# Kernel tuning notes

Hardware: AMD Instinct MI355X
Metric: run time of the kernel (lower is better)

## Reference

```python
import jax, jax.numpy as jnp
import numpy as np
from jax import lax

N = 51200            # total nodes
E = 409600           # edges
FEAT = 768           # BERT emb size
HID = 256            # GGNN out_channels
L = 6                # GGNN layers
NPG = 200            # nodes per graph (conv1d_1 in_channels)
C1_OUT, K1, P1 = 50, 3, 1
C2_OUT, K2 = 20, 1
MP1_K, MP1_S = 3, 2
MP2_K, MP2_S = 2, 2

def _pooled_len(n):
    n = (n - MP1_K) // MP1_S + 1
    n = (n - MP2_K) // MP2_S + 1
    return n

def setup_inputs():
    key = jax.random.key(0)
    ks = jax.random.split(key, 12)
    s = lambda i, shape: jax.random.normal(ks[i], shape, jnp.float32) * 0.02
    fc1_in = C2_OUT * _pooled_len(HID + FEAT)  # 20*255 = 5100
    fc2_in = C2_OUT * _pooled_len(HID)         # 20*63  = 1260
    return dict(
        x=jax.random.normal(ks[0], (N, FEAT), jnp.float32),
        edge_index=jax.random.randint(ks[1], (2, E), 0, N, dtype=jnp.int32),
        W_in=s(2, (HID, FEAT)), b_in=jnp.zeros((HID,), jnp.float32),
        W_ggnn=s(3, (L, HID, HID)),
        W_ih=s(4, (3 * HID, HID)), W_hh=s(5, (3 * HID, HID)),
        b_ih=jnp.zeros((3 * HID,), jnp.float32), b_hh=jnp.zeros((3 * HID,), jnp.float32),
        Wc1=s(6, (C1_OUT, NPG, K1)), bc1=jnp.zeros((C1_OUT,), jnp.float32),
        Wc2=s(7, (C2_OUT, C1_OUT, K2)), bc2=jnp.zeros((C2_OUT,), jnp.float32),
        Wf1=s(8, (1, fc1_in)), bf1=jnp.zeros((1,), jnp.float32),
        Wf2=s(9, (1, fc2_in)), bf2=jnp.zeros((1,), jnp.float32),
    )

def _conv1d(x, w, b, pad):
    y = lax.conv_general_dilated(x, w, (1,), [(pad, pad)], dimension_numbers=('NCH', 'OIH', 'NCH'))
    return y + b[None, :, None]

def _maxpool1d(x, k, s):
    return lax.reduce_window(x, -jnp.inf, lax.max, (1, 1, k), (1, 1, s), 'VALID')

def _ggnn(h0, src, dst, W_ggnn, W_ih, W_hh, b_ih, b_hh):
    h = h0
    for i in range(L):  # fixed small layer loop
        m = h @ W_ggnn[i]                                   # [N, HID]
        agg = jax.ops.segment_sum(m[src], dst, num_segments=N)  # scatter-add aggr
        gi = agg @ W_ih.T + b_ih                            # GRUCell input gates
        gh = h @ W_hh.T + b_hh                              # GRUCell hidden gates
        i_r, i_z, i_n = jnp.split(gi, 3, axis=1)
        h_r, h_z, h_n = jnp.split(gh, 3, axis=1)
        r = jax.nn.sigmoid(i_r + h_r)
        z = jax.nn.sigmoid(i_z + h_z)
        n = jnp.tanh(i_n + r * h_n)
        h = (1.0 - z) * n + z * h
    return h

def _conv_head(h, x, Wc1, bc1, Wc2, bc2, Wf1, bf1, Wf2, bf2):
    concat = jnp.concatenate([h, x], axis=1).reshape(-1, NPG, HID + FEAT)  # [G, NPG, 1024]
    Z = _maxpool1d(jax.nn.relu(_conv1d(concat, Wc1, bc1, P1)), MP1_K, MP1_S)
    Z = _maxpool1d(_conv1d(Z, Wc2, bc2, 0), MP2_K, MP2_S)
    Y = h.reshape(-1, NPG, HID)
    Y = _maxpool1d(jax.nn.relu(_conv1d(Y, Wc1, bc1, P1)), MP1_K, MP1_S)
    Y = _maxpool1d(_conv1d(Y, Wc2, bc2, 0), MP2_K, MP2_S)
    z = Z.reshape(Z.shape[0], -1) @ Wf1.T + bf1
    y = Y.reshape(Y.shape[0], -1) @ Wf2.T + bf2
    # dropout p=0.2 is identity in eval mode
    return jax.nn.sigmoid((z * y).ravel())  # [G]

def reference(x, edge_index, W_in, b_in, W_ggnn, W_ih, W_hh, b_ih, b_hh, Wc1, bc1, Wc2, bc2, Wf1, bf1, Wf2, bf2):
    h0 = x @ W_in.T + b_in
    h = _ggnn(h0, edge_index[0], edge_index[1], W_ggnn, W_ih, W_hh, b_ih, b_hh)
    p = _conv_head(h, x, Wc1, bc1, Wc2, bc2, Wf1, bf1, Wf2, bf2)
    eps = 1e-6
    p = jnp.clip(p, eps, 1.0 - eps)
    z1 = jnp.log(p / (1.0 - p))
    return jnp.stack([jnp.zeros_like(z1), z1], axis=1)  # [G, 2]
```

## Files before the change

### kernel.cpp

```cpp
#include <hip/hip_runtime.h>
#include <math.h>

#define N_NODES 51200
#define N_EDGES 409600
#define FEAT    768
#define HID     256
#define NPG     200
#define G_GRAPHS 256

typedef _Float16 f16x8 __attribute__((ext_vector_type(8)));
typedef _Float16 f16x4 __attribute__((ext_vector_type(4)));
typedef float    f32x4 __attribute__((ext_vector_type(4)));

__device__ __forceinline__ void cvt4(const float* __restrict__ in, _Float16* __restrict__ out, int i) {
    float4 v = *(const float4*)&in[i * 4];
    f16x4 h;
    h[0] = (_Float16)v.x; h[1] = (_Float16)v.y; h[2] = (_Float16)v.z; h[3] = (_Float16)v.w;
    *(f16x4*)&out[i * 4] = h;
}

__global__ __launch_bounds__(256) void k_prep(const float* __restrict__ W_in, const float* __restrict__ W_ih,
                                              const float* __restrict__ W_hh, const float* __restrict__ W_g,
                                              const float* __restrict__ x, const float* __restrict__ Wc1,
                                              const float* __restrict__ bih, const float* __restrict__ bhh,
                                              _Float16* __restrict__ Win_h, _Float16* __restrict__ Wih_h,
                                              _Float16* __restrict__ Whh_h, _Float16* __restrict__ Wg_h,
                                              _Float16* __restrict__ XF, _Float16* __restrict__ Wp,
                                              float* __restrict__ brz, float* __restrict__ bnn,
                                              _Float16* __restrict__ Wrz2,
                                              int* __restrict__ deg, int* __restrict__ fill) {
    int id = blockIdx.x * 256 + threadIdx.x;
    if (id < 49152) { cvt4(W_in, Win_h, id); return; }
    id -= 49152;
    if (id < 49152) { cvt4(W_ih, Wih_h, id); return; }
    id -= 49152;
    if (id < 49152) { cvt4(W_hh, Whh_h, id); return; }
    id -= 49152;
    if (id < 98304) { cvt4(W_g, Wg_h, id); return; }
    id -= 98304;
    if (id < 49152) {
        int ch = id / 12288, r = id - ch * 12288;
        int o = r / 192, k = r - o * 192;
        int dk = k >> 6, cc = k & 63;
        int c = ch * 64 + cc;
        float v = 0.f;
        if (o < 50 && c < NPG) v = Wc1[(o * NPG + c) * 3 + dk];
        Wp[id] = (_Float16)v;
        return;
    }
    id -= 49152;
    if (id < 1024) {
        if (id < 512) brz[id] = bih[id] + bhh[id];
        else {
            int q = id - 512;
            bnn[q] = (q < 256) ? bih[512 + q] : bhh[512 + (q - 256)];
        }
        return;
    }
    id -= 1024;
    if (id < 786432) {
        int l = id >> 17, r = id & 131071;
        int j = r >> 8, c = r & 255;
        Wrz2[(size_t)l * 262144 + j * 512 + 256 + c] = (_Float16)W_hh[j * 256 + c];
        return;
    }
    id -= 786432;
    if (id < 12800) { *(int4*)&deg[id * 4] = make_int4(0, 0, 0, 0); return; }
    id -= 12800;
    if (id < 12800) { *(int4*)&fill[id * 4] = make_int4(0, 0, 0, 0); return; }
    id -= 12800;
    if (id < 9830400) { cvt4(x, XF, id); return; }
}

__global__ __launch_bounds__(256) void k_deg(const int* __restrict__ ei, int* __restrict__ deg) {
    int e = blockIdx.x * 256 + threadIdx.x;
    if (e < N_EDGES) atomicAdd(&deg[ei[N_EDGES + e]], 1);
}

__global__ __launch_bounds__(1024) void k_scan(const int* __restrict__ deg, int* __restrict__ rowp) {
    __shared__ int sums[1024];
    int tid = threadIdx.x;
    int base = tid * 50;
    int s = 0;
    for (int j = 0; j < 50; ++j) s += deg[base + j];
    sums[tid] = s;
    __syncthreads();
    for (int off = 1; off < 1024; off <<= 1) {
        int v = 0;
        if (tid >= off) v = sums[tid - off];
        __syncthreads();
        sums[tid] += v;
        __syncthreads();
    }
    int run = sums[tid] - s;
    for (int j = 0; j < 50; ++j) { rowp[base + j] = run; run += deg[base + j]; }
    if (tid == 1023) rowp[N_NODES] = run;
}

__global__ __launch_bounds__(256) void k_fill(const int* __restrict__ ei, const int* __restrict__ rowp,
                                              int* __restrict__ fill, int* __restrict__ col) {
    int e = blockIdx.x * 256 + threadIdx.x;
    if (e < N_EDGES) {
        int d = ei[N_EDGES + e];
        int pos = atomicAdd(&fill[d], 1);
        col[rowp[d] + pos] = ei[e];
    }
}

template<int AF16, int OUT, int COLB, int SWZ>
__global__ __launch_bounds__(256) void k_gemm2(const void* __restrict__ Av, int lda,
                                               const _Float16* __restrict__ B,
                                               const float* __restrict__ bias,
                                               void* __restrict__ Cv, int ldc,
                                               int K, int wgPerL, int aLStride, int bLStride,
                                               int cLStride, int biasStride) {
    __shared__ _Float16 As[128 * 64];
    __shared__ _Float16 Bs[128 * 64];
    int wg = blockIdx.x;
    int l = wg / wgPerL; wg -= l * wgPerL;
    if (AF16) Av = (const void*)((const _Float16*)Av + (size_t)l * aLStride);
    else      Av = (const void*)((const float*)Av + (size_t)l * aLStride);
    B += (size_t)l * bLStride;
    if (bias) bias += (size_t)l * biasStride;
    if (OUT == 1) Cv = (void*)((_Float16*)Cv + (size_t)l * cLStride);
    else          Cv = (void*)((float*)Cv + (size_t)l * cLStride);
    int rowBase, colBase;
    if (SWZ) {
        int xcd = wg & 7, t = wg >> 3;
        int cb = t % COLB, gidx = t / COLB;
        rowBase = (gidx * 8 + xcd) * 128;
        colBase = cb * 128;
    } else {
        rowBase = (wg / COLB) * 128;
        colBase = (wg % COLB) * 128;
    }
    int tid = threadIdx.x;
    int lane = tid & 63;
    int wid = tid >> 6;
    int wr = wid >> 1, wc = wid & 1;
    f32x4 acc[4][4] = {};
    for (int k0 = 0; k0 < K; k0 += 64) {
        __syncthreads();
        #pragma unroll
        for (int p = 0; p < 4; ++p) {
            int c = p * 256 + tid;
            int row = c >> 3, slot = c & 7;
            int dst = row * 64 + ((slot ^ (row & 7)) * 8);
            if (AF16) {
                const _Float16* srcA = (const _Float16*)Av + (size_t)(rowBase + row) * lda + k0 + slot * 8;
                *(f16x8*)&As[dst] = *(const f16x8*)srcA;
            } else {
                const float* srcA = (const float*)Av + (size_t)(rowBase + row) * lda + k0 + slot * 8;
                float4 f0 = *(const float4*)srcA;
                float4 f1 = *(const float4*)(srcA + 4);
                f16x8 hv;
                hv[0] = (_Float16)f0.x; hv[1] = (_Float16)f0.y; hv[2] = (_Float16)f0.z; hv[3] = (_Float16)f0.w;
                hv[4] = (_Float16)f1.x; hv[5] = (_Float16)f1.y; hv[6] = (_Float16)f1.z; hv[7] = (_Float16)f1.w;
                *(f16x8*)&As[dst] = hv;
            }
            const _Float16* srcB = B + (size_t)(colBase + row) * K + k0 + slot * 8;
            *(f16x8*)&Bs[dst] = *(const f16x8*)srcB;
        }
        __syncthreads();
        #pragma unroll
        for (int ks = 0; ks < 2; ++ks) {
            f16x8 af[4], bf[4];
            #pragma unroll
            for (int mi = 0; mi < 4; ++mi) {
                int row = wr * 64 + mi * 16 + (lane & 15);
                int slot = (lane >> 4) + ks * 4;
                af[mi] = *(const f16x8*)&As[row * 64 + ((slot ^ (row & 7)) * 8)];
            }
            #pragma unroll
            for (int nj = 0; nj < 4; ++nj) {
                int row = wc * 64 + nj * 16 + (lane & 15);
                int slot = (lane >> 4) + ks * 4;
                bf[nj] = *(const f16x8*)&Bs[row * 64 + ((slot ^ (row & 7)) * 8)];
            }
            #pragma unroll
            for (int mi = 0; mi < 4; ++mi)
                #pragma unroll
                for (int nj = 0; nj < 4; ++nj)
                    acc[mi][nj] = __builtin_amdgcn_mfma_f32_16x16x32_f16(af[mi], bf[nj], acc[mi][nj], 0, 0, 0);
        }
    }
    #pragma unroll
    for (int mi = 0; mi < 4; ++mi) {
        #pragma unroll
        for (int nj = 0; nj < 4; ++nj) {
            int col = colBase + wc * 64 + nj * 16 + (lane & 15);
            float bv = bias ? bias[col] : 0.f;
            #pragma unroll
            for (int r = 0; r < 4; ++r) {
                int row = rowBase + wr * 64 + mi * 16 + (lane >> 4) * 4 + r;
                float val = acc[mi][nj][r] + bv;
                if (OUT == 0) ((float*)Cv)[(size_t)row * ldc + col] = val;
                else          ((_Float16*)Cv)[(size_t)row * ldc + col] = (_Float16)val;
            }
        }
    }
}

__global__ __launch_bounds__(256) void k_gemmrz(const _Float16* __restrict__ S, const _Float16* __restrict__ hc,
                                                const _Float16* __restrict__ B, const float* __restrict__ bias,
                                                _Float16* __restrict__ C) {
    __shared__ _Float16 As[128 * 64];
    __shared__ _Float16 Bs[128 * 64];
    int wg = blockIdx.x;
    int xcd = wg & 7, t = wg >> 3;
    int cb = t % 4, gidx = t / 4;
    int rowBase = (gidx * 8 + xcd) * 128;
    int colBase = cb * 128;
    int tid = threadIdx.x;
    int lane = tid & 63;
    int wid = tid >> 6;
    int wr = wid >> 1, wc = wid & 1;
    f32x4 acc[4][4] = {};
    for (int k0 = 0; k0 < 512; k0 += 64) {
        const _Float16* Abase = (k0 < 256) ? S : hc;
        int kk = k0 & 255;
        __syncthreads();
        #pragma unroll
        for (int p = 0; p < 4; ++p) {
            int c = p * 256 + tid;
            int row = c >> 3, slot = c & 7;
            int dst = row * 64 + ((slot ^ (row & 7)) * 8);
            *(f16x8*)&As[dst] = *(const f16x8*)&Abase[(size_t)(rowBase + row) * 256 + kk + slot * 8];
            *(f16x8*)&Bs[dst] = *(const f16x8*)&B[(size_t)(colBase + row) * 512 + k0 + slot * 8];
        }
        __syncthreads();
        #pragma unroll
        for (int ks = 0; ks < 2; ++ks) {
            f16x8 af[4], bf[4];
            #pragma unroll
            for (int mi = 0; mi < 4; ++mi) {
                int row = wr * 64 + mi * 16 + (lane & 15);
                int slot = (lane >> 4) + ks * 4;
                af[mi] = *(const f16x8*)&As[row * 64 + ((slot ^ (row & 7)) * 8)];
            }
            #pragma unroll
            for (int nj = 0; nj < 4; ++nj) {
                int row = wc * 64 + nj * 16 + (lane & 15);
                int slot = (lane >> 4) + ks * 4;
                bf[nj] = *(const f16x8*)&Bs[row * 64 + ((slot ^ (row & 7)) * 8)];
            }
            #pragma unroll
            for (int mi = 0; mi < 4; ++mi)
                #pragma unroll
                for (int nj = 0; nj < 4; ++nj)
                    acc[mi][nj] = __builtin_amdgcn_mfma_f32_16x16x32_f16(af[mi], bf[nj], acc[mi][nj], 0, 0, 0);
        }
    }
    #pragma unroll
    for (int mi = 0; mi < 4; ++mi) {
        #pragma unroll
        for (int nj = 0; nj < 4; ++nj) {
            int col = colBase + wc * 64 + nj * 16 + (lane & 15);
            float bv = bias[col];
            #pragma unroll
            for (int r = 0; r < 4; ++r) {
                int row = rowBase + wr * 64 + mi * 16 + (lane >> 4) * 4 + r;
                C[(size_t)row * 512 + col] = (_Float16)(acc[mi][nj][r] + bv);
            }
        }
    }
}

__global__ __launch_bounds__(512) void k_nngru(const _Float16* __restrict__ S, const _Float16* __restrict__ hc,
                                               const _Float16* __restrict__ B0, const _Float16* __restrict__ B1,
                                               const float* __restrict__ bnn, const _Float16* __restrict__ rz,
                                               _Float16* __restrict__ hn) {
    __shared__ _Float16 As0[128 * 64], As1[128 * 64], Bs0[128 * 64], Bs1[128 * 64];
    int wg = blockIdx.x;
    int xcd = wg & 7, t = wg >> 3;
    int cb = t % 2, gidx = t / 2;
    int rowBase = (gidx * 8 + xcd) * 128;
    int colBase = cb * 128;
    int tid = threadIdx.x;
    int lane = tid & 63;
    int wid = tid >> 6;
    int wr = wid >> 2, wc = wid & 3;
    f32x4 acc0[4][2] = {}, acc1[4][2] = {};
    for (int k0 = 0; k0 < 256; k0 += 64) {
        __syncthreads();
        #pragma unroll
        for (int p = 0; p < 8; ++p) {
            int q = p * 512 + tid;
            int tile = q >> 10;
            int c = q & 1023;
            int row = c >> 3, slot = c & 7;
            int dst = row * 64 + ((slot ^ (row & 7)) * 8);
            const _Float16* src;
            _Float16* d;
            if (tile == 0)      { src = S  + (size_t)(rowBase + row) * 256 + k0 + slot * 8; d = As0; }
            else if (tile == 1) { src = hc + (size_t)(rowBase + row) * 256 + k0 + slot * 8; d = As1; }
            else if (tile == 2) { src = B0 + (size_t)(colBase + row) * 256 + k0 + slot * 8; d = Bs0; }
            else                { src = B1 + (size_t)(colBase + row) * 256 + k0 + slot * 8; d = Bs1; }
            *(f16x8*)&d[dst] = *(const f16x8*)src;
        }
        __syncthreads();
        #pragma unroll
        for (int ks = 0; ks < 2; ++ks) {
            f16x8 a0[4], a1[4], b0[2], b1[2];
            #pragma unroll
            for (int mi = 0; mi < 4; ++mi) {
                int row = wr * 64 + mi * 16 + (lane & 15);
                int slot = (lane >> 4) + ks * 4;
                int off = row * 64 + ((slot ^ (row & 7)) * 8);
                a0[mi] = *(const f16x8*)&As0[off];
                a1[mi] = *(const f16x8*)&As1[off];
            }
            #pragma unroll
            for (int nj = 0; nj < 2; ++nj) {
                int row = wc * 32 + nj * 16 + (lane & 15);
                int slot = (lane >> 4) + ks * 4;
                int off = row * 64 + ((slot ^ (row & 7)) * 8);
                b0[nj] = *(const f16x8*)&Bs0[off];
                b1[nj] = *(const f16x8*)&Bs1[off];
            }
            #pragma unroll
            for (int mi = 0; mi < 4; ++mi)
                #pragma unroll
                for (int nj = 0; nj < 2; ++nj) {
                    acc0[mi][nj] = __builtin_amdgcn_mfma_f32_16x16x32_f16(a0[mi], b0[nj], acc0[mi][nj], 0, 0, 0);
                    acc1[mi][nj] = __builtin_amdgcn_mfma_f32_16x16x32_f16(a1[mi], b1[nj], acc1[mi][nj], 0, 0, 0);
                }
        }
    }
    #pragma unroll
    for (int mi = 0; mi < 4; ++mi) {
        #pragma unroll
        for (int nj = 0; nj < 2; ++nj) {
            int col = colBase + wc * 32 + nj * 16 + (lane & 15);
            float bi = bnn[col], bh = bnn[256 + col];
            #pragma unroll
            for (int r = 0; r < 4; ++r) {
                int row = rowBase + wr * 64 + mi * 16 + (lane >> 4) * 4 + r;
                float rv = (float)rz[(size_t)row * 512 + col];
                float zv = (float)rz[(size_t)row * 512 + 256 + col];
                float rg = 1.f / (1.f + expf(-rv));
                float zg = 1.f / (1.f + expf(-zv));
                float ng = tanhf((acc0[mi][nj][r] + bi) + rg * (acc1[mi][nj][r] + bh));
                float ho = (float)hc[(size_t)row * 256 + col];
                hn[(size_t)row * 256 + col] = (_Float16)((1.f - zg) * ng + zg * ho);
            }
        }
    }
}

__global__ __launch_bounds__(256) void k_agg5(const int* __restrict__ rowp, const int* __restrict__ col,
                                              const _Float16* __restrict__ hc, _Float16* __restrict__ S) {
    int v = blockIdx.x * 8 + (threadIdx.x >> 5);
    int lane = threadIdx.x & 31;
    int beg = rowp[v], end = rowp[v + 1];
    const _Float16* hf = hc + lane * 8;
    float a0 = 0.f, a1 = 0.f, a2 = 0.f, a3 = 0.f, a4 = 0.f, a5 = 0.f, a6 = 0.f, a7 = 0.f;
    int i = beg;
    for (; i + 3 < end; i += 4) {
        int c0 = col[i], c1 = col[i + 1], c2 = col[i + 2], c3 = col[i + 3];
        f16x8 u0 = *(const f16x8*)&hf[(size_t)c0 * 256];
        f16x8 u1 = *(const f16x8*)&hf[(size_t)c1 * 256];
        f16x8 u2 = *(const f16x8*)&hf[(size_t)c2 * 256];
        f16x8 u3 = *(const f16x8*)&hf[(size_t)c3 * 256];
        a0 += ((float)u0[0] + (float)u1[0]) + ((float)u2[0] + (float)u3[0]);
        a1 += ((float)u0[1] + (float)u1[1]) + ((float)u2[1] + (float)u3[1]);
        a2 += ((float)u0[2] + (float)u1[2]) + ((float)u2[2] + (float)u3[2]);
        a3 += ((float)u0[3] + (float)u1[3]) + ((float)u2[3] + (float)u3[3]);
        a4 += ((float)u0[4] + (float)u1[4]) + ((float)u2[4] + (float)u3[4]);
        a5 += ((float)u0[5] + (float)u1[5]) + ((float)u2[5] + (float)u3[5]);
        a6 += ((float)u0[6] + (float)u1[6]) + ((float)u2[6] + (float)u3[6]);
        a7 += ((float)u0[7] + (float)u1[7]) + ((float)u2[7] + (float)u3[7]);
    }
    for (; i < end; ++i) {
        f16x8 u = *(const f16x8*)&hf[(size_t)col[i] * 256];
        a0 += (float)u[0]; a1 += (float)u[1]; a2 += (float)u[2]; a3 += (float)u[3];
        a4 += (float)u[4]; a5 += (float)u[5]; a6 += (float)u[6]; a7 += (float)u[7];
    }
    f16x8 o;
    o[0] = (_Float16)a0; o[1] = (_Float16)a1; o[2] = (_Float16)a2; o[3] = (_Float16)a3;
    o[4] = (_Float16)a4; o[5] = (_Float16)a5; o[6] = (_Float16)a6; o[7] = (_Float16)a7;
    *(f16x8*)&S[(size_t)v * 256 + lane * 8] = o;
}

__global__ __launch_bounds__(256, 2) void k_conv1m(const _Float16* __restrict__ hf, const _Float16* __restrict__ xf,
                                                   const _Float16* __restrict__ Wp, const float* __restrict__ bc1,
                                                   float* __restrict__ outZ, float* __restrict__ outY) {
    __shared__ _Float16 XT[272 * 64];
    __shared__ _Float16 WL[64 * 192];
    int b = blockIdx.x;
    int g, t0, H;
    float* out;
    if (b < 1024) { g = b >> 2; t0 = (b & 3) * 256; H = 1024; out = outZ; }
    else          { g = b - 1024; t0 = 0; H = 256; out = outY; }
    int tid = threadIdx.x;
    int lane = tid & 63;
    int wn = (tid >> 6) * 64;
    f32x4 acc[4][4] = {};
    for (int ch = 0; ch < 4; ++ch) {
        __syncthreads();
        #pragma unroll
        for (int i = 0; i < 6; ++i) {
            int q = i * 256 + tid;
            int o = q / 24, sk = q - o * 24;
            int skp = (sk & 0x18) | ((sk & 7) ^ (o & 7));
            *(f16x8*)&WL[o * 192 + skp * 8] = *(const f16x8*)&Wp[ch * 12288 + o * 192 + sk * 8];
        }
        for (int u = tid; u < 272; u += 256) {
            int r8 = u / 34, pc = u - r8 * 34;
            int gstart = t0 - 8 + pc * 8;
            int c0 = r8 * 8;
            f16x8 zv;
            #pragma unroll
            for (int q = 0; q < 8; ++q) zv[q] = (_Float16)0.f;
            f16x8 rows[8];
            if (gstart < 0 || gstart >= H) {
                #pragma unroll
                for (int j = 0; j < 8; ++j) rows[j] = zv;
            } else {
                const _Float16* base;
                int stride;
                if (gstart < HID) { base = hf + gstart; stride = 256; }
                else              { base = xf + (gstart - HID); stride = 768; }
                int node0 = g * NPG + ch * 64 + c0;
                #pragma unroll
                for (int j = 0; j < 8; ++j) {
                    int cg = ch * 64 + c0 + j;
                    rows[j] = (cg < NPG) ? *(const f16x8*)&base[(size_t)(node0 + j) * stride] : zv;
                }
            }
            #pragma unroll
            for (int jj = 0; jj < 8; ++jj) {
                f16x8 w;
                #pragma unroll
                for (int j = 0; j < 8; ++j) w[j] = rows[j][jj];
                int p = pc * 8 + jj;
                int slot = r8 ^ jj ^ (pc & 7);
                *(f16x8*)&XT[p * 64 + slot * 8] = w;
            }
        }
        __syncthreads();
        #pragma unroll
        for (int ks = 0; ks < 6; ++ks) {
            int dk = ks >> 1, cs0 = (ks & 1) << 2;
            f16x8 af[4], bf[4];
            #pragma unroll
            for (int mi = 0; mi < 4; ++mi) {
                int o = mi * 16 + (lane & 15);
                int sk = ks * 4 + (lane >> 4);
                int skp = (sk & 0x18) | ((sk & 7) ^ (o & 7));
                af[mi] = *(const f16x8*)&WL[o * 192 + skp * 8];
            }
            #pragma unroll
            for (int nj = 0; nj < 4; ++nj) {
                int tw = wn + nj * 16 + (lane & 15) + dk + 7;
                int sp = (cs0 + (lane >> 4)) ^ (tw & 7) ^ ((tw >> 3) & 7);
                bf[nj] = *(const f16x8*)&XT[tw * 64 + sp * 8];
            }
            #pragma unroll
            for (int mi = 0; mi < 4; ++mi)
                #pragma unroll
                for (int nj = 0; nj < 4; ++nj)
                    acc[mi][nj] = __builtin_amdgcn_mfma_f32_16x16x32_f16(af[mi], bf[nj], acc[mi][nj], 0, 0, 0);
        }
    }
    #pragma unroll
    for (int mi = 0; mi < 4; ++mi) {
        #pragma unroll
        for (int r = 0; r < 4; ++r) {
            int o = mi * 16 + (lane >> 4) * 4 + r;
            if (o < 50) {
                float bv = bc1[o];
                #pragma unroll
                for (int nj = 0; nj < 4; ++nj) {
                    int t = t0 + wn + nj * 16 + (lane & 15);
                    float v = acc[mi][nj][r] + bv;
                    out[(size_t)g * 50 * H + (size_t)o * H + t] = v > 0.f ? v : 0.f;
                }
            }
        }
    }
}

__global__ __launch_bounds__(256) void k_pool1(const float* __restrict__ C1Z, const float* __restrict__ C1Y,
                                               float* __restrict__ P1Z, float* __restrict__ P1Y) {
    int b = blockIdx.x;
    const float* in;
    float* out;
    int H, U, go;
    if (b < 12800) { in = C1Z; out = P1Z; H = 1024; U = 511; go = b; }
    else           { in = C1Y; out = P1Y; H = 256;  U = 127; go = b - 12800; }
    const float* p = in + (size_t)go * H;
    float* q = out + (size_t)go * U;
    for (int u = threadIdx.x; u < U; u += 256) {
        float a = p[2 * u], bb = p[2 * u + 1], c = p[2 * u + 2];
        float mm = a > bb ? a : bb;
        q[u] = mm > c ? mm : c;
    }
}

__global__ __launch_bounds__(256) void k_c2p2(const float* __restrict__ P1Z, const float* __restrict__ P1Y,
                                              const float* __restrict__ Wc2, const float* __restrict__ bc2,
                                              float* __restrict__ P2Z, float* __restrict__ P2Y) {
    int g = blockIdx.x, oy = blockIdx.y;
    const float* P1;
    float* out;
    int U, U2, o2;
    if (oy < 20) { P1 = P1Z; out = P2Z; U = 511; U2 = 255; o2 = oy; }
    else         { P1 = P1Y; out = P2Y; U = 127; U2 = 63;  o2 = oy - 20; }
    float b = bc2[o2];
    for (int u2 = threadIdx.x; u2 < U2; u2 += 256) {
        float a0 = b, a1 = b;
        #pragma unroll 5
        for (int i = 0; i < 50; ++i) {
            float wv = Wc2[o2 * 50 + i];
            const float* p = P1 + ((size_t)g * 50 + i) * U + 2 * u2;
            a0 = fmaf(p[0], wv, a0);
            a1 = fmaf(p[1], wv, a1);
        }
        out[((size_t)g * 20 + o2) * U2 + u2] = a0 > a1 ? a0 : a1;
    }
}

__global__ __launch_bounds__(256) void k_fc(const float* __restrict__ P2Z, const float* __restrict__ P2Y,
                                            const float* __restrict__ Wf1, const float* __restrict__ bf1,
                                            const float* __restrict__ Wf2, const float* __restrict__ bf2,
                                            float* __restrict__ zb, float* __restrict__ yb) {
    __shared__ float red[256];
    int b = blockIdx.x, tid = threadIdx.x;
    int g = b & 255;
    const float* P2;
    const float* Wf;
    const float* bf;
    float* out;
    int len;
    if (b < 256) { P2 = P2Z; Wf = Wf1; bf = bf1; out = zb; len = 20 * 255; }
    else         { P2 = P2Y; Wf = Wf2; bf = bf2; out = yb; len = 20 * 63; }
    const float* p = P2 + (size_t)g * len;
    float s = 0.f;
    for (int i = tid; i < len; i += 256) s = fmaf(p[i], Wf[i], s);
    red[tid] = s;
    __syncthreads();
    for (int off = 128; off > 0; off >>= 1) {
        if (tid < off) red[tid] += red[tid + off];
        __syncthreads();
    }
    if (tid == 0) out[g] = red[0] + bf[0];
}

__global__ __launch_bounds__(256) void k_final(const float* __restrict__ z, const float* __restrict__ y,
                                               float* __restrict__ out) {
    int g = threadIdx.x;
    float t = z[g] * y[g];
    float p = 1.f / (1.f + expf(-t));
    p = fminf(fmaxf(p, 1e-6f), 1.f - 1e-6f);
    float z1 = logf(p / (1.f - p));
    out[2 * g] = 0.f;
    out[2 * g + 1] = z1;
}

extern "C" void kernel_launch(void* const* d_in, const int* in_sizes, int n_in,
                              void* d_out, int out_size, void* d_ws, size_t ws_size,
                              hipStream_t stream) {
    const float* x     = (const float*)d_in[0];
    const int*   ei    = (const int*)d_in[1];
    const float* W_in  = (const float*)d_in[2];
    const float* b_in  = (const float*)d_in[3];
    const float* W_g   = (const float*)d_in[4];
    const float* W_ih  = (const float*)d_in[5];
    const float* W_hh  = (const float*)d_in[6];
    const float* b_ih  = (const float*)d_in[7];
    const float* b_hh  = (const float*)d_in[8];
    const float* Wc1   = (const float*)d_in[9];
    const float* bc1   = (const float*)d_in[10];
    const float* Wc2   = (const float*)d_in[11];
    const float* bc2   = (const float*)d_in[12];
    const float* Wf1   = (const float*)d_in[13];
    const float* bf1   = (const float*)d_in[14];
    const float* Wf2   = (const float*)d_in[15];
    const float* bf2   = (const float*)d_in[16];

    float* ws = (float*)d_ws;
    const size_t OFF_S   = 0;
    const size_t OFF_HA  = 6553600;
    const size_t OFF_HB  = 13107200;
    const size_t OFF_RZ  = 19660800;
    const size_t OFF_XF  = 32768000;
    const size_t OFF_WF  = 52428800;
    const size_t OFF_BRZ = 53927936;
    const size_t OFF_BNN = 53928448;
    const size_t OFF_INT = 53928960;
    const size_t OFF_ZB  = 54492200;
    const size_t OFF_P2Z = 54500000;
    const size_t OFF_P2Y = 55900000;

    _Float16* S  = (_Float16*)(ws + OFF_S);
    _Float16* HA = (_Float16*)(ws + OFF_HA);
    _Float16* HB = (_Float16*)(ws + OFF_HB);
    _Float16* RZ = (_Float16*)(ws + OFF_RZ);
    _Float16* XF = (_Float16*)(ws + OFF_XF);

    _Float16* Win_h = (_Float16*)(ws + OFF_WF);
    _Float16* Wih_h = Win_h + 196608;
    _Float16* Whh_h = Wih_h + 196608;
    _Float16* Wg_h  = Whh_h + 196608;
    _Float16* Wrz2  = Wg_h  + 393216;
    _Float16* Wni2  = Wrz2  + 1572864;
    _Float16* Wp    = Wni2  + 393216;
    _Float16* Whhn  = Whh_h + 512 * 256;
    float* brz = ws + OFF_BRZ;
    float* bnn = ws + OFF_BNN;

    int* deg  = (int*)(ws + OFF_INT);
    int* fill = deg + N_NODES;
    int* rowp = fill + N_NODES;
    int* col  = rowp + (N_NODES + 1);
    float* zb = ws + OFF_ZB;
    float* yb = zb + 256;

    float* C1Z = ws + OFF_RZ;
    float* P1Z = ws + OFF_HB;
    float* C1Y = ws + OFF_S;
    float* P1Y = ws + 3300000;
    float* P2Z = ws + OFF_P2Z;
    float* P2Y = ws + OFF_P2Y;

    k_prep<<<42728, 256, 0, stream>>>(W_in, W_ih, W_hh, W_g, x, Wc1, b_ih, b_hh,
                                      Win_h, Wih_h, Whh_h, Wg_h, XF, Wp, brz, bnn, Wrz2,
                                      deg, fill);
    k_gemm2<1, 1, 2, 0><<<48, 256, 0, stream>>>(Wih_h, 256, Wg_h, nullptr,
                                                Wrz2, 512, 256, 8, 0, 65536, 262144, 0);
    k_gemm2<1, 1, 2, 0><<<24, 256, 0, stream>>>(Wih_h + 512 * 256, 256, Wg_h, nullptr,
                                                Wni2, 256, 256, 4, 0, 65536, 65536, 0);

    k_deg<<<N_EDGES / 256, 256, 0, stream>>>(ei, deg);
    k_scan<<<1, 1024, 0, stream>>>(deg, rowp);
    k_fill<<<N_EDGES / 256, 256, 0, stream>>>(ei, rowp, fill, col);

    k_gemm2<1, 1, 2, 1><<<800, 256, 0, stream>>>(XF, FEAT, Win_h, b_in, HA, HID,
                                                 FEAT, 800, 0, 0, 0, 0);

    for (int l = 0; l < 6; ++l) {
        _Float16* hc = (l & 1) ? HB : HA;
        _Float16* hn = (l & 1) ? HA : HB;
        k_agg5<<<6400, 256, 0, stream>>>(rowp, col, hc, S);
        k_gemmrz<<<1600, 256, 0, stream>>>(S, hc, Wrz2 + (size_t)l * 262144, brz, RZ);
        k_nngru<<<800, 512, 0, stream>>>(S, hc, Wni2 + (size_t)l * 65536, Whhn, bnn, RZ, hn);
    }

    k_conv1m<<<1280, 256, 0, stream>>>(HA, XF, Wp, bc1, C1Z, C1Y);
    k_pool1<<<25600, 256, 0, stream>>>(C1Z, C1Y, P1Z, P1Y);
    k_c2p2<<<dim3(G_GRAPHS, 40), 256, 0, stream>>>(P1Z, P1Y, Wc2, bc2, P2Z, P2Y);
    k_fc<<<512, 256, 0, stream>>>(P2Z, P2Y, Wf1, bf1, Wf2, bf2, zb, yb);

    k_final<<<1, 256, 0, stream>>>(zb, yb, (float*)d_out);
}
```

Before: 1.119 ms.

## Drop fp16 copy of x and fuse conv2, pooling, FC and final head

```diff
diff --git a/kernel.cpp b/kernel.cpp
--- a/kernel.cpp
+++ b/kernel.cpp
@@ -21,11 +21,11 @@
 
 __global__ __launch_bounds__(256) void k_prep(const float* __restrict__ W_in, const float* __restrict__ W_ih,
                                               const float* __restrict__ W_hh, const float* __restrict__ W_g,
-                                              const float* __restrict__ x, const float* __restrict__ Wc1,
+                                              const float* __restrict__ Wc1,
                                               const float* __restrict__ bih, const float* __restrict__ bhh,
                                               _Float16* __restrict__ Win_h, _Float16* __restrict__ Wih_h,
                                               _Float16* __restrict__ Whh_h, _Float16* __restrict__ Wg_h,
-                                              _Float16* __restrict__ XF, _Float16* __restrict__ Wp,
+                                              _Float16* __restrict__ Wp,
                                               float* __restrict__ brz, float* __restrict__ bnn,
                                               _Float16* __restrict__ Wrz2,
                                               int* __restrict__ deg, int* __restrict__ fill) {
@@ -68,8 +68,6 @@
     if (id < 12800) { *(int4*)&deg[id * 4] = make_int4(0, 0, 0, 0); return; }
     id -= 12800;
     if (id < 12800) { *(int4*)&fill[id * 4] = make_int4(0, 0, 0, 0); return; }
-    id -= 12800;
-    if (id < 9830400) { cvt4(x, XF, id); return; }
 }
 
 __global__ __launch_bounds__(256) void k_deg(const int* __restrict__ ei, int* __restrict__ deg) {
@@ -382,7 +380,7 @@
     *(f16x8*)&S[(size_t)v * 256 + lane * 8] = o;
 }
 
-__global__ __launch_bounds__(256, 2) void k_conv1m(const _Float16* __restrict__ hf, const _Float16* __restrict__ xf,
+__global__ __launch_bounds__(256, 2) void k_conv1m(const _Float16* __restrict__ hf, const float* __restrict__ xf,
                                                    const _Float16* __restrict__ Wp, const float* __restrict__ bc1,
                                                    float* __restrict__ outZ, float* __restrict__ outY) {
     __shared__ _Float16 XT[272 * 64];
@@ -416,16 +414,29 @@
             if (gstart < 0 || gstart >= H) {
                 #pragma unroll
                 for (int j = 0; j < 8; ++j) rows[j] = zv;
-            } else {
-                const _Float16* base;
-                int stride;
-                if (gstart < HID) { base = hf + gstart; stride = 256; }
-                else              { base = xf + (gstart - HID); stride = 768; }
+            } else if (gstart < HID) {
+                const _Float16* base = hf + gstart;
                 int node0 = g * NPG + ch * 64 + c0;
                 #pragma unroll
                 for (int j = 0; j < 8; ++j) {
                     int cg = ch * 64 + c0 + j;
-                    rows[j] = (cg < NPG) ? *(const f16x8*)&base[(size_t)(node0 + j) * stride] : zv;
+                    rows[j] = (cg < NPG) ? *(const f16x8*)&base[(size_t)(node0 + j) * 256] : zv;
+                }
+            } else {
+                const float* base = xf + (gstart - HID);
+                int node0 = g * NPG + ch * 64 + c0;
+                #pragma unroll
+                for (int j = 0; j < 8; ++j) {
+                    int cg = ch * 64 + c0 + j;
+                    if (cg < NPG) {
+                        const float* rp = base + (size_t)(node0 + j) * FEAT;
+                        float4 f0 = *(const float4*)rp;
+                        float4 f1 = *(const float4*)(rp + 4);
+                        f16x8 hv;
+                        hv[0] = (_Float16)f0.x; hv[1] = (_Float16)f0.y; hv[2] = (_Float16)f0.z; hv[3] = (_Float16)f0.w;
+                        hv[4] = (_Float16)f1.x; hv[5] = (_Float16)f1.y; hv[6] = (_Float16)f1.z; hv[7] = (_Float16)f1.w;
+                        rows[j] = hv;
+                    } else rows[j] = zv;
                 }
             }
             #pragma unroll
@@ -498,64 +509,78 @@
     }
 }
 
-__global__ __launch_bounds__(256) void k_c2p2(const float* __restrict__ P1Z, const float* __restrict__ P1Y,
+__global__ __launch_bounds__(256) void k_c2fc(const float* __restrict__ P1Z, const float* __restrict__ P1Y,
                                               const float* __restrict__ Wc2, const float* __restrict__ bc2,
-                                              float* __restrict__ P2Z, float* __restrict__ P2Y) {
-    int g = blockIdx.x, oy = blockIdx.y;
-    const float* P1;
-    float* out;
-    int U, U2, o2;
-    if (oy < 20) { P1 = P1Z; out = P2Z; U = 511; U2 = 255; o2 = oy; }
-    else         { P1 = P1Y; out = P2Y; U = 127; U2 = 63;  o2 = oy - 20; }
-    float b = bc2[o2];
-    for (int u2 = threadIdx.x; u2 < U2; u2 += 256) {
-        float a0 = b, a1 = b;
-        #pragma unroll 5
+                                              const float* __restrict__ Wf1, const float* __restrict__ bf1,
+                                              const float* __restrict__ Wf2, const float* __restrict__ bf2,
+                                              float* __restrict__ out) {
+    __shared__ float wL[20][52];
+    __shared__ float red[256];
+    int g = blockIdx.x, tid = threadIdx.x;
+    for (int l = tid; l < 1000; l += 256) wL[l / 50][l % 50] = Wc2[l];
+    __syncthreads();
+    float s = 0.f;
+    if (tid < 255) {
+        const float* p = P1Z + (size_t)g * 50 * 511 + 2 * tid;
+        float a0[20], a1[20];
+        #pragma unroll
+        for (int o = 0; o < 20; ++o) { a0[o] = bc2[o]; a1[o] = a0[o]; }
         for (int i = 0; i < 50; ++i) {
-            float wv = Wc2[o2 * 50 + i];
-            const float* p = P1 + ((size_t)g * 50 + i) * U + 2 * u2;
-            a0 = fmaf(p[0], wv, a0);
-            a1 = fmaf(p[1], wv, a1);
-        }
-        out[((size_t)g * 20 + o2) * U2 + u2] = a0 > a1 ? a0 : a1;
-    }
-}
-
-__global__ __launch_bounds__(256) void k_fc(const float* __restrict__ P2Z, const float* __restrict__ P2Y,
-                                            const float* __restrict__ Wf1, const float* __restrict__ bf1,
-                                            const float* __restrict__ Wf2, const float* __restrict__ bf2,
-                                            float* __restrict__ zb, float* __restrict__ yb) {
-    __shared__ float red[256];
-    int b = blockIdx.x, tid = threadIdx.x;
-    int g = b & 255;
-    const float* P2;
-    const float* Wf;
-    const float* bf;
-    float* out;
-    int len;
-    if (b < 256) { P2 = P2Z; Wf = Wf1; bf = bf1; out = zb; len = 20 * 255; }
-    else         { P2 = P2Y; Wf = Wf2; bf = bf2; out = yb; len = 20 * 63; }
-    const float* p = P2 + (size_t)g * len;
-    float s = 0.f;
-    for (int i = tid; i < len; i += 256) s = fmaf(p[i], Wf[i], s);
+            float p0 = p[(size_t)i * 511], p1 = p[(size_t)i * 511 + 1];
+            #pragma unroll
+            for (int o = 0; o < 20; ++o) {
+                a0[o] = fmaf(p0, wL[o][i], a0[o]);
+                a1[o] = fmaf(p1, wL[o][i], a1[o]);
+            }
+        }
+        #pragma unroll
+        for (int o = 0; o < 20; ++o) {
+            float m = a0[o] > a1[o] ? a0[o] : a1[o];
+            s = fmaf(m, Wf1[o * 255 + tid], s);
+        }
+    }
     red[tid] = s;
     __syncthreads();
     for (int off = 128; off > 0; off >>= 1) {
         if (tid < off) red[tid] += red[tid + off];
         __syncthreads();
     }
-    if (tid == 0) out[g] = red[0] + bf[0];
-}
-
-__global__ __launch_bounds__(256) void k_final(const float* __restrict__ z, const float* __restrict__ y,
-                                               float* __restrict__ out) {
-    int g = threadIdx.x;
-    float t = z[g] * y[g];
-    float p = 1.f / (1.f + expf(-t));
-    p = fminf(fmaxf(p, 1e-6f), 1.f - 1e-6f);
-    float z1 = logf(p / (1.f - p));
-    out[2 * g] = 0.f;
-    out[2 * g + 1] = z1;
+    float zv = red[0] + bf1[0];
+    __syncthreads();
+    s = 0.f;
+    if (tid < 63) {
+        const float* p = P1Y + (size_t)g * 50 * 127 + 2 * tid;
+        float a0[20], a1[20];
+        #pragma unroll
+        for (int o = 0; o < 20; ++o) { a0[o] = bc2[o]; a1[o] = a0[o]; }
+        for (int i = 0; i < 50; ++i) {
+            float p0 = p[(size_t)i * 127], p1 = p[(size_t)i * 127 + 1];
+            #pragma unroll
+            for (int o = 0; o < 20; ++o) {
+                a0[o] = fmaf(p0, wL[o][i], a0[o]);
+                a1[o] = fmaf(p1, wL[o][i], a1[o]);
+            }
+        }
+        #pragma unroll
+        for (int o = 0; o < 20; ++o) {
+            float m = a0[o] > a1[o] ? a0[o] : a1[o];
+            s = fmaf(m, Wf2[o * 63 + tid], s);
+        }
+    }
+    red[tid] = s;
+    __syncthreads();
+    for (int off = 128; off > 0; off >>= 1) {
+        if (tid < off) red[tid] += red[tid + off];
+        __syncthreads();
+    }
+    if (tid == 0) {
+        float yv = red[0] + bf2[0];
+        float t = zv * yv;
+        float pp = 1.f / (1.f + expf(-t));
+        pp = fminf(fmaxf(pp, 1e-6f), 1.f - 1e-6f);
+        out[2 * g] = 0.f;
+        out[2 * g + 1] = logf(pp / (1.f - pp));
+    }
 }
 
 extern "C" void kernel_launch(void* const* d_in, const int* in_sizes, int n_in,
@@ -584,20 +609,15 @@
     const size_t OFF_HA  = 6553600;
     const size_t OFF_HB  = 13107200;
     const size_t OFF_RZ  = 19660800;
-    const size_t OFF_XF  = 32768000;
     const size_t OFF_WF  = 52428800;
     const size_t OFF_BRZ = 53927936;
     const size_t OFF_BNN = 53928448;
     const size_t OFF_INT = 53928960;
-    const size_t OFF_ZB  = 54492200;
-    const size_t OFF_P2Z = 54500000;
-    const size_t OFF_P2Y = 55900000;
 
     _Float16* S  = (_Float16*)(ws + OFF_S);
     _Float16* HA = (_Float16*)(ws + OFF_HA);
     _Float16* HB = (_Float16*)(ws + OFF_HB);
     _Float16* RZ = (_Float16*)(ws + OFF_RZ);
-    _Float16* XF = (_Float16*)(ws + OFF_XF);
 
     _Float16* Win_h = (_Float16*)(ws + OFF_WF);
     _Float16* Wih_h = Win_h + 196608;
@@ -614,19 +634,15 @@
     int* fill = deg + N_NODES;
     int* rowp = fill + N_NODES;
     int* col  = rowp + (N_NODES + 1);
-    float* zb = ws + OFF_ZB;
-    float* yb = zb + 256;
 
     float* C1Z = ws + OFF_RZ;
     float* P1Z = ws + OFF_HB;
     float* C1Y = ws + OFF_S;
     float* P1Y = ws + 3300000;
-    float* P2Z = ws + OFF_P2Z;
-    float* P2Y = ws + OFF_P2Y;
-
-    k_prep<<<42728, 256, 0, stream>>>(W_in, W_ih, W_hh, W_g, x, Wc1, b_ih, b_hh,
-                                      Win_h, Wih_h, Whh_h, Wg_h, XF, Wp, brz, bnn, Wrz2,
-                                      deg, fill);
+
+    k_prep<<<4328, 256, 0, stream>>>(W_in, W_ih, W_hh, W_g, Wc1, b_ih, b_hh,
+                                     Win_h, Wih_h, Whh_h, Wg_h, Wp, brz, bnn, Wrz2,
+                                     deg, fill);
     k_gemm2<1, 1, 2, 0><<<48, 256, 0, stream>>>(Wih_h, 256, Wg_h, nullptr,
                                                 Wrz2, 512, 256, 8, 0, 65536, 262144, 0);
     k_gemm2<1, 1, 2, 0><<<24, 256, 0, stream>>>(Wih_h + 512 * 256, 256, Wg_h, nullptr,
@@ -636,7 +652,7 @@
     k_scan<<<1, 1024, 0, stream>>>(deg, rowp);
     k_fill<<<N_EDGES / 256, 256, 0, stream>>>(ei, rowp, fill, col);
 
-    k_gemm2<1, 1, 2, 1><<<800, 256, 0, stream>>>(XF, FEAT, Win_h, b_in, HA, HID,
+    k_gemm2<0, 1, 2, 1><<<800, 256, 0, stream>>>(x, FEAT, Win_h, b_in, HA, HID,
                                                  FEAT, 800, 0, 0, 0, 0);
 
     for (int l = 0; l < 6; ++l) {
@@ -647,10 +663,7 @@
         k_nngru<<<800, 512, 0, stream>>>(S, hc, Wni2 + (size_t)l * 65536, Whhn, bnn, RZ, hn);
     }
 
-    k_conv1m<<<1280, 256, 0, stream>>>(HA, XF, Wp, bc1, C1Z, C1Y);
+    k_conv1m<<<1280, 256, 0, stream>>>(HA, x, Wp, bc1, C1Z, C1Y);
     k_pool1<<<25600, 256, 0, stream>>>(C1Z, C1Y, P1Z, P1Y);
-    k_c2p2<<<dim3(G_GRAPHS, 40), 256, 0, stream>>>(P1Z, P1Y, Wc2, bc2, P2Z, P2Y);
-    k_fc<<<512, 256, 0, stream>>>(P2Z, P2Y, Wf1, bf1, Wf2, bf2, zb, yb);
-
-    k_final<<<1, 256, 0, stream>>>(zb, yb, (float*)d_out);
-}
+    k_c2fc<<<G_GRAPHS, 256, 0, stream>>>(P1Z, P1Y, Wc2, bc2, Wf1, bf1, Wf2, bf2, (float*)d_out);
+}
```

Result: no change. 1.135 ms (+1.4%).
